# Kernel tuning notes

Measured on AMD Instinct MI355X. Metric: run time of the kernel, lower is better.

The kernel has to match this reference:

```python
import jax, jax.numpy as jnp
import numpy as np

TOP_K = 2


def setup_inputs() -> dict:
    key = jax.random.key(0)
    k1, k2, k3, k4, k5 = jax.random.split(key, 5)
    B, S, H, F, E = 4, 2048, 1024, 4096, 8
    scale = 1.0 / np.sqrt(H)
    return {
        "hidden_states": jax.random.normal(k1, (B, S, H), dtype=jnp.float32),
        "gate_w": jax.random.normal(k2, (E, H), dtype=jnp.float32) * scale,
        "w1": jax.random.normal(k3, (E, F, H), dtype=jnp.float32) * scale,
        "w3": jax.random.normal(k4, (E, F, H), dtype=jnp.float32) * scale,
        "w2": jax.random.normal(k5, (E, H, F), dtype=jnp.float32) * (1.0 / np.sqrt(F)),
    }


def reference(hidden_states, gate_w, w1, w3, w2):
    B, S, H = hidden_states.shape
    E = gate_w.shape[0]
    x = hidden_states.reshape(-1, H)                    # [T, H], T = B*S

    router_logits = x @ gate_w.T                        # [T, E]
    probs = jax.nn.softmax(router_logits.astype(jnp.float32), axis=-1)
    top_w, top_i = jax.lax.top_k(probs, TOP_K)          # [T, k]
    top_w = top_w / jnp.sum(top_w, axis=-1, keepdims=True)
    top_w = top_w.astype(x.dtype)

    # combine weight of each expert for each token: [E, T]
    one_hot = jax.nn.one_hot(top_i, E, dtype=x.dtype)   # [T, k, E]
    comb = jnp.einsum("tke,tk->et", one_hot, top_w)

    # loop over experts via scan; tokens not routed to expert e have comb==0,
    # which matches the gather/FFN/scatter-combine of the original exactly.
    def body(acc, wts):
        w1e, w3e, w2e, ce = wts
        h = jax.nn.silu(x @ w1e.T) * (x @ w3e.T)        # [T, F]
        return acc + (h @ w2e.T) * ce[:, None], None

    out0 = jnp.zeros_like(x)
    out, _ = jax.lax.scan(body, out0, (w1, w3, w2, comb))
    return out.reshape(B, S, H), router_logits
```

## Files before the change

kernel.cpp:

```cpp
#include <hip/hip_runtime.h>
#include <hip/hip_bf16.h>

#define T_TOK 8192
#define HDIM  1024
#define FDIM  4096
#define NEXP  8
#define CVT_BLKS 1024

typedef __attribute__((ext_vector_type(8))) short short8;
typedef __attribute__((ext_vector_type(4))) float f32x4;
typedef unsigned short u16;
typedef unsigned int   u32;

#define XB_OFF    0ull
#define W1B_OFF   (XB_OFF   + 16777216ull)
#define W3B_OFF   (W1B_OFF  + 67108864ull)
#define W2B_OFF   (W3B_OFF  + 67108864ull)
#define HBUF_OFF  (W2B_OFF  + 67108864ull)
#define CNT_OFF   (HBUF_OFF + 134217728ull)
#define TLIST_OFF (CNT_OFF  + 128ull)
#define WLIST_OFF (TLIST_OFF + 262144ull)
#define WS_NEED   (WLIST_OFF + 262144ull)

__device__ __forceinline__ u16 f2bf(float f) {
  u32 u = __float_as_uint(f);
  return (u16)((u + 0x7fffu + ((u >> 16) & 1u)) >> 16);
}
__device__ __forceinline__ float bf2f(u16 v) {
  return __uint_as_float((u32)v << 16);
}

__device__ __forceinline__ void gl_lds16(const void* g, void* l) {
  __builtin_amdgcn_global_load_lds(
      (const __attribute__((address_space(1))) void*)g,
      (__attribute__((address_space(3))) void*)l, 16, 0, 0);
}

__global__ __launch_bounds__(256) void prep_kernel(
    const float* __restrict__ x, const float* __restrict__ gw,
    const float* __restrict__ s0, const float* __restrict__ s1,
    u16* __restrict__ d0, u16* __restrict__ d1,
    float* __restrict__ logits, u16* __restrict__ xb,
    int* __restrict__ counts, int* __restrict__ tlist,
    float* __restrict__ wt1, float* __restrict__ wt2,
    int* __restrict__ slot1, int* __restrict__ slot2) {
  if (blockIdx.x < 8192) {
    const int n8 = NEXP * FDIM * HDIM / 8;
    const int total = 2 * n8;
    const int stride = 8192 * 256;
    for (int i = blockIdx.x * 256 + threadIdx.x; i < total; i += stride) {
      int seg = i >> 22;
      int j = i & (n8 - 1);
      const float* s = seg == 0 ? s0 : s1;
      u16* d = seg == 0 ? d0 : d1;
      float4 v0 = ((const float4*)s)[j * 2];
      float4 v1 = ((const float4*)s)[j * 2 + 1];
      uint4 o;
      o.x = (u32)f2bf(v0.x) | ((u32)f2bf(v0.y) << 16);
      o.y = (u32)f2bf(v0.z) | ((u32)f2bf(v0.w) << 16);
      o.z = (u32)f2bf(v1.x) | ((u32)f2bf(v1.y) << 16);
      o.w = (u32)f2bf(v1.z) | ((u32)f2bf(v1.w) << 16);
      ((uint4*)d)[j] = o;
    }
    return;
  }
  const int wid = threadIdx.x >> 6, lane = threadIdx.x & 63;
  const int t = (blockIdx.x - 8192) * 4 + wid;
  const float* xr = x + (size_t)t * HDIM + lane * 16;
  float4 xv[4];
#pragma unroll
  for (int q = 0; q < 4; ++q) xv[q] = ((const float4*)xr)[q];

  u32 pk[8];
#pragma unroll
  for (int q = 0; q < 4; ++q) {
    pk[q * 2 + 0] = (u32)f2bf(xv[q].x) | ((u32)f2bf(xv[q].y) << 16);
    pk[q * 2 + 1] = (u32)f2bf(xv[q].z) | ((u32)f2bf(xv[q].w) << 16);
  }
  u32* xbo = (u32*)(xb + (size_t)t * HDIM + lane * 16);
  ((uint4*)xbo)[0] = make_uint4(pk[0], pk[1], pk[2], pk[3]);
  ((uint4*)xbo)[1] = make_uint4(pk[4], pk[5], pk[6], pk[7]);

  float lg[NEXP];
#pragma unroll
  for (int e = 0; e < NEXP; ++e) {
    const float4* g = (const float4*)(gw + (size_t)e * HDIM + lane * 16);
    float s = 0.f;
#pragma unroll
    for (int q = 0; q < 4; ++q) {
      float4 gv = g[q];
      s += xv[q].x * gv.x + xv[q].y * gv.y + xv[q].z * gv.z + xv[q].w * gv.w;
    }
#pragma unroll
    for (int off = 32; off > 0; off >>= 1) s += __shfl_xor(s, off, 64);
    lg[e] = s;
  }
  if (lane == 0) {
    float* lo = logits + (size_t)t * NEXP;
#pragma unroll
    for (int e = 0; e < NEXP; ++e) lo[e] = lg[e];
    float v1 = -1e30f, v2 = -1e30f; int i1 = 0, i2 = 0;
#pragma unroll
    for (int e = 0; e < NEXP; ++e) {
      float le = lg[e];
      if (le > v1)      { v2 = v1; i2 = i1; v1 = le; i1 = e; }
      else if (le > v2) { v2 = le; i2 = e; }
    }
    float t2 = __expf(v2 - v1);
    float rs = 1.f / (1.f + t2);
    int p1 = atomicAdd(&counts[i1], 1);
    tlist[i1 * T_TOK + p1] = t;
    slot1[t] = (i1 << 16) | p1;  wt1[t] = rs;
    int p2 = atomicAdd(&counts[i2], 1);
    tlist[i2 * T_TOK + p2] = t;
    slot2[t] = (i2 << 16) | p2;  wt2[t] = t2 * rs;
  }
}

__global__ __launch_bounds__(512, 4) void ffn1_kernel(
    const u16* __restrict__ xb, const u16* __restrict__ w1b, const u16* __restrict__ w3b,
    u16* __restrict__ hbuf, const int* __restrict__ counts, const int* __restrict__ tlist,
    const float* __restrict__ w2src, u16* __restrict__ w2b) {
  if (blockIdx.x < CVT_BLKS) {
    const int n8 = NEXP * HDIM * FDIM / 8;
    const int stride = CVT_BLKS * 512;
    for (int j = blockIdx.x * 512 + threadIdx.x; j < n8; j += stride) {
      float4 v0 = ((const float4*)w2src)[j * 2];
      float4 v1 = ((const float4*)w2src)[j * 2 + 1];
      uint4 o;
      o.x = (u32)f2bf(v0.x) | ((u32)f2bf(v0.y) << 16);
      o.y = (u32)f2bf(v0.z) | ((u32)f2bf(v0.w) << 16);
      o.z = (u32)f2bf(v1.x) | ((u32)f2bf(v1.y) << 16);
      o.w = (u32)f2bf(v1.z) | ((u32)f2bf(v1.w) << 16);
      ((uint4*)w2b)[j] = o;
    }
    return;
  }
  const int bid = blockIdx.x - CVT_BLKS;
  const int e  = bid & 7;
  const int j  = bid >> 3;
  const int ct = j >> 6;
  const int rt = j & 63;
  const int Ne = counts[e];
  if (rt * 128 >= Ne) return;
  int hb = 0;
#pragma unroll
  for (int i = 0; i < NEXP; ++i) hb += (i < e) ? counts[i] : 0;

  __shared__ u16 LDS[24576];

  const int tid = threadIdx.x;
  const int wid = tid >> 6, lane = tid & 63;
  const int tset = wid >> 2;
  const int patch = wid & 3;
  const int wr = patch >> 1, wc = patch & 1;
  const int lr = lane & 15, lhi = lane >> 4;

  size_t aoff[2];
#pragma unroll
  for (int q = 0; q < 2; ++q) {
    int idx = q * 512 + tid;
    int r = idx >> 3, c = idx & 7;
    int grow = rt * 128 + r;
    int gi = grow < Ne ? grow : Ne - 1;
    aoff[q] = (size_t)tlist[e * T_TOK + gi] * HDIM + (size_t)((c ^ (r & 7)) * 8);
  }
  size_t boff[2];
#pragma unroll
  for (int q = 0; q < 2; ++q) {
    int idx = q * 512 + tid;
    int r = idx >> 3, c = idx & 7;
    boff[q] = ((size_t)e * FDIM + ct * 128 + r) * HDIM + (size_t)((c ^ (r & 7)) * 8);
  }
  const int dW = wid * 512;

  f32x4 acc[4][4] = {};
  const int bbase = 8192 + tset * 8192;

  for (int k0 = 0; k0 < HDIM; k0 += 64) {
    __syncthreads();
#pragma unroll
    for (int q = 0; q < 2; ++q) {
      gl_lds16(xb  + aoff[q] + k0, LDS + q * 4096 + dW);
      gl_lds16(w1b + boff[q] + k0, LDS + 8192 + q * 4096 + dW);
      gl_lds16(w3b + boff[q] + k0, LDS + 16384 + q * 4096 + dW);
    }
    __syncthreads();
#pragma unroll
    for (int kk = 0; kk < 2; ++kk) {
      const int chn = ((kk * 4 + lhi) ^ (lr & 7)) * 8;
      short8 af[4], bf_[4];
#pragma unroll
      for (int m = 0; m < 4; ++m)
        af[m] = *(const short8*)(LDS + (wr * 64 + m * 16 + lr) * 64 + chn);
#pragma unroll
      for (int n = 0; n < 4; ++n)
        bf_[n] = *(const short8*)(LDS + bbase + (wc * 64 + n * 16 + lr) * 64 + chn);
#pragma unroll
      for (int m = 0; m < 4; ++m)
#pragma unroll
        for (int n = 0; n < 4; ++n)
          acc[m][n] = __builtin_amdgcn_mfma_f32_16x16x32_bf16(af[m], bf_[n], acc[m][n], 0, 0, 0);
    }
  }

  __syncthreads();
  if (tset == 1) {
#pragma unroll
    for (int m = 0; m < 4; ++m)
#pragma unroll
      for (int n = 0; n < 4; ++n)
#pragma unroll
        for (int i = 0; i < 4; ++i)
          LDS[patch * 4096 + (m * 16 + lhi * 4 + i) * 64 + n * 16 + lr] = f2bf(acc[m][n][i]);
  }
  __syncthreads();
  if (tset == 0) {
    const int rbase = rt * 128 + wr * 64 + lhi * 4;
    const int cbase = ct * 128 + wc * 64 + lr;
#pragma unroll
    for (int m = 0; m < 4; ++m)
#pragma unroll
      for (int i = 0; i < 4; ++i) {
        int grow = rbase + m * 16 + i;
        if (grow < Ne) {
          size_t rowp = (size_t)(hb + grow) * FDIM + cbase;
#pragma unroll
          for (int n = 0; n < 4; ++n) {
            float a1 = acc[m][n][i];
            float a3 = bf2f(LDS[patch * 4096 + (m * 16 + lhi * 4 + i) * 64 + n * 16 + lr]);
            hbuf[rowp + n * 16] = f2bf((a1 / (1.f + __expf(-a1))) * a3);
          }
        }
      }
  }
}

__global__ __launch_bounds__(256, 4) void ffn2_kernel(
    const u16* __restrict__ hbuf, const u16* __restrict__ w2b,
    u16* __restrict__ ybuf, const int* __restrict__ counts) {
  const int bid = blockIdx.x;
  const int e  = bid & 7;
  const int j  = bid >> 3;
  const int ct = j >> 6;
  const int rt = j & 63;
  const int Ne = counts[e];
  if (rt * 128 >= Ne) return;
  int hb = 0;
#pragma unroll
  for (int i = 0; i < NEXP; ++i) hb += (i < e) ? counts[i] : 0;

  __shared__ u16 Alds[128 * 64];
  __shared__ u16 Blds[128 * 64];

  const int tid = threadIdx.x;
  const int wid = tid >> 6, lane = tid & 63;
  const int wr = wid >> 1, wc = wid & 1;
  const int lr = lane & 15, lhi = lane >> 4;

  size_t aoff[4], boff[4]; int ldso[4];
#pragma unroll
  for (int q = 0; q < 4; ++q) {
    int i = wid * 4 + q;
    int r = i * 8 + (lane >> 3);
    int sw = ((lane & 7) ^ (r & 7)) * 8;
    int grow = rt * 128 + r;
    int gi = grow < Ne ? grow : Ne - 1;
    aoff[q] = (size_t)(hb + gi) * FDIM + sw;
    int hr = ct * 128 + r;
    boff[q] = ((size_t)e * HDIM + hr) * FDIM + sw;
    ldso[q] = i * 512;
  }

  f32x4 acc[4][4] = {};

  for (int k0 = 0; k0 < FDIM; k0 += 64) {
    __syncthreads();
#pragma unroll
    for (int q = 0; q < 4; ++q) {
      gl_lds16(hbuf + aoff[q] + k0, Alds + ldso[q]);
      gl_lds16(w2b + boff[q] + k0, Blds + ldso[q]);
    }
    __syncthreads();
#pragma unroll
    for (int kk = 0; kk < 2; ++kk) {
      const int swo = ((kk * 4 + lhi) ^ (lr & 7)) * 8;
      short8 af[4], bf_[4];
#pragma unroll
      for (int m = 0; m < 4; ++m)
        af[m] = *(const short8*)(Alds + (wr * 64 + m * 16 + lr) * 64 + swo);
#pragma unroll
      for (int n = 0; n < 4; ++n)
        bf_[n] = *(const short8*)(Blds + (wc * 64 + n * 16 + lr) * 64 + swo);
#pragma unroll
      for (int m = 0; m < 4; ++m)
#pragma unroll
        for (int n = 0; n < 4; ++n)
          acc[m][n] = __builtin_amdgcn_mfma_f32_16x16x32_bf16(af[m], bf_[n], acc[m][n], 0, 0, 0);
    }
  }

  const int rb = rt * 128 + wr * 64 + lhi * 4;
  const int cb = ct * 128 + wc * 64 + lr;
#pragma unroll
  for (int m = 0; m < 4; ++m)
#pragma unroll
    for (int i = 0; i < 4; ++i) {
      int grow = rb + m * 16 + i;
      if (grow < Ne) {
        u16* yp = ybuf + (size_t)(hb + grow) * HDIM + cb;
#pragma unroll
        for (int n = 0; n < 4; ++n)
          yp[n * 16] = f2bf(acc[m][n][i]);
      }
    }
}

__global__ __launch_bounds__(256) void combine_kernel(
    const u16* __restrict__ ybuf, const int* __restrict__ slot1, const int* __restrict__ slot2,
    const float* __restrict__ wt1, const float* __restrict__ wt2,
    const int* __restrict__ counts, float* __restrict__ out) {
  int pre[NEXP + 1];
  pre[0] = 0;
#pragma unroll
  for (int i = 0; i < NEXP; ++i) pre[i + 1] = pre[i] + counts[i];
  int idx = blockIdx.x * 256 + threadIdx.x;
  int t = idx >> 7, c8 = (idx & 127) * 8;
  int s1 = slot1[t], s2 = slot2[t];
  float w1 = wt1[t], w2 = wt2[t];
  size_t r1 = (size_t)(pre[s1 >> 16] + (s1 & 0xFFFF)) * HDIM + c8;
  size_t r2 = (size_t)(pre[s2 >> 16] + (s2 & 0xFFFF)) * HDIM + c8;
  short8 y1 = *(const short8*)(ybuf + r1);
  short8 y2 = *(const short8*)(ybuf + r2);
  float* op = out + (size_t)t * HDIM + c8;
#pragma unroll
  for (int k = 0; k < 8; ++k)
    op[k] = w1 * bf2f((u16)y1[k]) + w2 * bf2f((u16)y2[k]);
}

extern "C" void kernel_launch(void* const* d_in, const int* in_sizes, int n_in,
                              void* d_out, int out_size, void* d_ws, size_t ws_size,
                              hipStream_t stream) {
  (void)in_sizes; (void)n_in; (void)out_size;
  if (ws_size < WS_NEED) return;

  const float* x  = (const float*)d_in[0];
  const float* gw = (const float*)d_in[1];
  const float* w1 = (const float*)d_in[2];
  const float* w3 = (const float*)d_in[3];
  const float* w2 = (const float*)d_in[4];
  float* out = (float*)d_out;
  float* logits = out + (size_t)T_TOK * HDIM;

  char* ws = (char*)d_ws;
  u16* xb    = (u16*)(ws + XB_OFF);
  u16* w1b   = (u16*)(ws + W1B_OFF);
  u16* w3b   = (u16*)(ws + W3B_OFF);
  u16* w2b   = (u16*)(ws + W2B_OFF);
  u16* hbuf  = (u16*)(ws + HBUF_OFF);
  u16* ybuf  = (u16*)(ws + W1B_OFF);
  int* counts = (int*)(ws + CNT_OFF);
  int* tlist  = (int*)(ws + TLIST_OFF);
  float* wt1  = (float*)(ws + WLIST_OFF);
  float* wt2  = wt1 + T_TOK;
  int* slot1  = (int*)(wt2 + T_TOK);
  int* slot2  = slot1 + T_TOK;

  hipMemsetAsync(counts, 0, NEXP * sizeof(int), stream);

  prep_kernel<<<8192 + 2048, 256, 0, stream>>>(x, gw, w1, w3, w1b, w3b,
                                               logits, xb, counts, tlist,
                                               wt1, wt2, slot1, slot2);
  ffn1_kernel<<<CVT_BLKS + NEXP * 64 * 32, 512, 0, stream>>>(
      xb, w1b, w3b, hbuf, counts, tlist, w2, w2b);
  ffn2_kernel<<<NEXP * 64 * 8, 256, 0, stream>>>(hbuf, w2b, ybuf, counts);
  combine_kernel<<<T_TOK * 128 / 256, 256, 0, stream>>>(ybuf, slot1, slot2, wt1, wt2, counts, out);
}
```

Baseline: 844.6 us.

## Retile FFN GEMMs so each wave computes both gate and up products

```diff
diff --git a/kernel.cpp b/kernel.cpp
--- a/kernel.cpp
+++ b/kernel.cpp
@@ -5,7 +5,7 @@
 #define HDIM  1024
 #define FDIM  4096
 #define NEXP  8
-#define CVT_BLKS 1024
+#define CVT_BLKS 2048
 
 typedef __attribute__((ext_vector_type(8))) short short8;
 typedef __attribute__((ext_vector_type(4))) float f32x4;
@@ -117,14 +117,14 @@
   }
 }
 
-__global__ __launch_bounds__(512, 4) void ffn1_kernel(
+__global__ __launch_bounds__(256, 2) void ffn1_kernel(
     const u16* __restrict__ xb, const u16* __restrict__ w1b, const u16* __restrict__ w3b,
     u16* __restrict__ hbuf, const int* __restrict__ counts, const int* __restrict__ tlist,
     const float* __restrict__ w2src, u16* __restrict__ w2b) {
   if (blockIdx.x < CVT_BLKS) {
     const int n8 = NEXP * HDIM * FDIM / 8;
-    const int stride = CVT_BLKS * 512;
-    for (int j = blockIdx.x * 512 + threadIdx.x; j < n8; j += stride) {
+    const int stride = CVT_BLKS * 256;
+    for (int j = blockIdx.x * 256 + threadIdx.x; j < n8; j += stride) {
       float4 v0 = ((const float4*)w2src)[j * 2];
       float4 v1 = ((const float4*)w2src)[j * 2 + 1];
       uint4 o;
@@ -151,92 +151,76 @@
 
   const int tid = threadIdx.x;
   const int wid = tid >> 6, lane = tid & 63;
-  const int tset = wid >> 2;
-  const int patch = wid & 3;
-  const int wr = patch >> 1, wc = patch & 1;
+  const int wc = wid;
   const int lr = lane & 15, lhi = lane >> 4;
 
-  size_t aoff[2];
-#pragma unroll
-  for (int q = 0; q < 2; ++q) {
-    int idx = q * 512 + tid;
+  size_t aoff[4], b1off[4], b3off[4];
+#pragma unroll
+  for (int q = 0; q < 4; ++q) {
+    int idx = q * 256 + tid;
     int r = idx >> 3, c = idx & 7;
+    int sw = (c ^ (r & 7)) * 8;
     int grow = rt * 128 + r;
     int gi = grow < Ne ? grow : Ne - 1;
-    aoff[q] = (size_t)tlist[e * T_TOK + gi] * HDIM + (size_t)((c ^ (r & 7)) * 8);
-  }
-  size_t boff[2];
-#pragma unroll
-  for (int q = 0; q < 2; ++q) {
-    int idx = q * 512 + tid;
-    int r = idx >> 3, c = idx & 7;
-    boff[q] = ((size_t)e * FDIM + ct * 128 + r) * HDIM + (size_t)((c ^ (r & 7)) * 8);
+    aoff[q]  = (size_t)tlist[e * T_TOK + gi] * HDIM + sw;
+    b1off[q] = ((size_t)e * FDIM + ct * 128 + r) * HDIM + sw;
+    b3off[q] = b1off[q];
   }
   const int dW = wid * 512;
 
-  f32x4 acc[4][4] = {};
-  const int bbase = 8192 + tset * 8192;
+  f32x4 acc1[8][2] = {}, acc3[8][2] = {};
 
   for (int k0 = 0; k0 < HDIM; k0 += 64) {
     __syncthreads();
 #pragma unroll
-    for (int q = 0; q < 2; ++q) {
-      gl_lds16(xb  + aoff[q] + k0, LDS + q * 4096 + dW);
-      gl_lds16(w1b + boff[q] + k0, LDS + 8192 + q * 4096 + dW);
-      gl_lds16(w3b + boff[q] + k0, LDS + 16384 + q * 4096 + dW);
+    for (int q = 0; q < 4; ++q) {
+      gl_lds16(xb  + aoff[q]  + k0, LDS + q * 2048 + dW);
+      gl_lds16(w1b + b1off[q] + k0, LDS + 8192 + q * 2048 + dW);
+      gl_lds16(w3b + b3off[q] + k0, LDS + 16384 + q * 2048 + dW);
     }
     __syncthreads();
 #pragma unroll
     for (int kk = 0; kk < 2; ++kk) {
       const int chn = ((kk * 4 + lhi) ^ (lr & 7)) * 8;
-      short8 af[4], bf_[4];
-#pragma unroll
-      for (int m = 0; m < 4; ++m)
-        af[m] = *(const short8*)(LDS + (wr * 64 + m * 16 + lr) * 64 + chn);
-#pragma unroll
-      for (int n = 0; n < 4; ++n)
-        bf_[n] = *(const short8*)(LDS + bbase + (wc * 64 + n * 16 + lr) * 64 + chn);
-#pragma unroll
-      for (int m = 0; m < 4; ++m)
-#pragma unroll
-        for (int n = 0; n < 4; ++n)
-          acc[m][n] = __builtin_amdgcn_mfma_f32_16x16x32_bf16(af[m], bf_[n], acc[m][n], 0, 0, 0);
-    }
-  }
-
-  __syncthreads();
-  if (tset == 1) {
-#pragma unroll
-    for (int m = 0; m < 4; ++m)
-#pragma unroll
-      for (int n = 0; n < 4; ++n)
-#pragma unroll
-        for (int i = 0; i < 4; ++i)
-          LDS[patch * 4096 + (m * 16 + lhi * 4 + i) * 64 + n * 16 + lr] = f2bf(acc[m][n][i]);
-  }
-  __syncthreads();
-  if (tset == 0) {
-    const int rbase = rt * 128 + wr * 64 + lhi * 4;
-    const int cbase = ct * 128 + wc * 64 + lr;
-#pragma unroll
-    for (int m = 0; m < 4; ++m)
-#pragma unroll
-      for (int i = 0; i < 4; ++i) {
-        int grow = rbase + m * 16 + i;
-        if (grow < Ne) {
-          size_t rowp = (size_t)(hb + grow) * FDIM + cbase;
-#pragma unroll
-          for (int n = 0; n < 4; ++n) {
-            float a1 = acc[m][n][i];
-            float a3 = bf2f(LDS[patch * 4096 + (m * 16 + lhi * 4 + i) * 64 + n * 16 + lr]);
-            hbuf[rowp + n * 16] = f2bf((a1 / (1.f + __expf(-a1))) * a3);
-          }
+      short8 af[8], b1f[2], b3f[2];
+#pragma unroll
+      for (int m = 0; m < 8; ++m)
+        af[m] = *(const short8*)(LDS + (m * 16 + lr) * 64 + chn);
+#pragma unroll
+      for (int n = 0; n < 2; ++n) {
+        int ro = (wc * 32 + n * 16 + lr) * 64 + chn;
+        b1f[n] = *(const short8*)(LDS + 8192 + ro);
+        b3f[n] = *(const short8*)(LDS + 16384 + ro);
+      }
+#pragma unroll
+      for (int m = 0; m < 8; ++m)
+#pragma unroll
+        for (int n = 0; n < 2; ++n) {
+          acc1[m][n] = __builtin_amdgcn_mfma_f32_16x16x32_bf16(af[m], b1f[n], acc1[m][n], 0, 0, 0);
+          acc3[m][n] = __builtin_amdgcn_mfma_f32_16x16x32_bf16(af[m], b3f[n], acc3[m][n], 0, 0, 0);
+        }
+    }
+  }
+
+  const int rbase = rt * 128 + lhi * 4;
+  const int cbase = ct * 128 + wc * 32 + lr;
+#pragma unroll
+  for (int m = 0; m < 8; ++m)
+#pragma unroll
+    for (int i = 0; i < 4; ++i) {
+      int grow = rbase + m * 16 + i;
+      if (grow < Ne) {
+        size_t rowp = (size_t)(hb + grow) * FDIM + cbase;
+#pragma unroll
+        for (int n = 0; n < 2; ++n) {
+          float a1 = acc1[m][n][i], a3 = acc3[m][n][i];
+          hbuf[rowp + n * 16] = f2bf((a1 / (1.f + __expf(-a1))) * a3);
         }
       }
-  }
-}
-
-__global__ __launch_bounds__(256, 4) void ffn2_kernel(
+    }
+}
+
+__global__ __launch_bounds__(256, 2) void ffn2_kernel(
     const u16* __restrict__ hbuf, const u16* __restrict__ w2b,
     u16* __restrict__ ybuf, const int* __restrict__ counts) {
   const int bid = blockIdx.x;
@@ -250,63 +234,67 @@
 #pragma unroll
   for (int i = 0; i < NEXP; ++i) hb += (i < e) ? counts[i] : 0;
 
-  __shared__ u16 Alds[128 * 64];
-  __shared__ u16 Blds[128 * 64];
+  __shared__ u16 LDS[24576];
 
   const int tid = threadIdx.x;
   const int wid = tid >> 6, lane = tid & 63;
-  const int wr = wid >> 1, wc = wid & 1;
+  const int wc = wid;
   const int lr = lane & 15, lhi = lane >> 4;
 
-  size_t aoff[4], boff[4]; int ldso[4];
+  size_t aoff[4], boff[8];
 #pragma unroll
   for (int q = 0; q < 4; ++q) {
-    int i = wid * 4 + q;
-    int r = i * 8 + (lane >> 3);
-    int sw = ((lane & 7) ^ (r & 7)) * 8;
+    int idx = q * 256 + tid;
+    int r = idx >> 3, c = idx & 7;
+    int sw = (c ^ (r & 7)) * 8;
     int grow = rt * 128 + r;
     int gi = grow < Ne ? grow : Ne - 1;
     aoff[q] = (size_t)(hb + gi) * FDIM + sw;
-    int hr = ct * 128 + r;
-    boff[q] = ((size_t)e * HDIM + hr) * FDIM + sw;
-    ldso[q] = i * 512;
-  }
-
-  f32x4 acc[4][4] = {};
+  }
+#pragma unroll
+  for (int q = 0; q < 8; ++q) {
+    int idx = q * 256 + tid;
+    int r = idx >> 3, c = idx & 7;
+    boff[q] = ((size_t)e * HDIM + ct * 256 + r) * FDIM + (size_t)((c ^ (r & 7)) * 8);
+  }
+  const int dW = wid * 512;
+
+  f32x4 acc[8][4] = {};
 
   for (int k0 = 0; k0 < FDIM; k0 += 64) {
     __syncthreads();
 #pragma unroll
-    for (int q = 0; q < 4; ++q) {
-      gl_lds16(hbuf + aoff[q] + k0, Alds + ldso[q]);
-      gl_lds16(w2b + boff[q] + k0, Blds + ldso[q]);
-    }
+    for (int q = 0; q < 4; ++q)
+      gl_lds16(hbuf + aoff[q] + k0, LDS + q * 2048 + dW);
+#pragma unroll
+    for (int q = 0; q < 8; ++q)
+      gl_lds16(w2b + boff[q] + k0, LDS + 8192 + q * 2048 + dW);
     __syncthreads();
 #pragma unroll
     for (int kk = 0; kk < 2; ++kk) {
-      const int swo = ((kk * 4 + lhi) ^ (lr & 7)) * 8;
-      short8 af[4], bf_[4];
-#pragma unroll
-      for (int m = 0; m < 4; ++m)
-        af[m] = *(const short8*)(Alds + (wr * 64 + m * 16 + lr) * 64 + swo);
+      const int chn = ((kk * 4 + lhi) ^ (lr & 7)) * 8;
+      short8 af[8], bf_[4];
+#pragma unroll
+      for (int m = 0; m < 8; ++m)
+        af[m] = *(const short8*)(LDS + (m * 16 + lr) * 64 + chn);
 #pragma unroll
       for (int n = 0; n < 4; ++n)
-        bf_[n] = *(const short8*)(Blds + (wc * 64 + n * 16 + lr) * 64 + swo);
-#pragma unroll
-      for (int m = 0; m < 4; ++m)
+        bf_[n] = *(const short8*)(LDS + 8192 + (wc * 64 + n * 16 + lr) * 64 + chn);
+#pragma unroll
+      for (int m = 0; m < 8; ++m)
 #pragma unroll
         for (int n = 0; n < 4; ++n)
           acc[m][n] = __builtin_amdgcn_mfma_f32_16x16x32_bf16(af[m], bf_[n], acc[m][n], 0, 0, 0);
     }
   }
 
-  const int rb = rt * 128 + wr * 64 + lhi * 4;
-  const int cb = ct * 128 + wc * 64 + lr;
-#pragma unroll
-  for (int m = 0; m < 4; ++m)
+  const int rbase = rt * 128 + lhi * 4;
+  const int cb = ct * 256 + wc * 64 + lr;
+#pragma unroll
+  for (int m = 0; m < 8; ++m)
 #pragma unroll
     for (int i = 0; i < 4; ++i) {
-      int grow = rb + m * 16 + i;
+      int grow = rbase + m * 16 + i;
       if (grow < Ne) {
         u16* yp = ybuf + (size_t)(hb + grow) * HDIM + cb;
 #pragma unroll
@@ -371,8 +359,8 @@
   prep_kernel<<<8192 + 2048, 256, 0, stream>>>(x, gw, w1, w3, w1b, w3b,
                                                logits, xb, counts, tlist,
                                                wt1, wt2, slot1, slot2);
-  ffn1_kernel<<<CVT_BLKS + NEXP * 64 * 32, 512, 0, stream>>>(
+  ffn1_kernel<<<CVT_BLKS + NEXP * 64 * 32, 256, 0, stream>>>(
       xb, w1b, w3b, hbuf, counts, tlist, w2, w2b);
-  ffn2_kernel<<<NEXP * 64 * 8, 256, 0, stream>>>(hbuf, w2b, ybuf, counts);
+  ffn2_kernel<<<NEXP * 64 * 4, 256, 0, stream>>>(hbuf, w2b, ybuf, counts);
   combine_kernel<<<T_TOK * 128 / 256, 256, 0, stream>>>(ybuf, slot1, slot2, wt1, wt2, counts, out);
 }
```

Result: slower. 866.6 us (+2.6%).
